# Optimization experiments

Measured on AMD Instinct MI355X. Metric: run time of the kernel, lower is better.

Reference implementation:

```python
import jax, jax.numpy as jnp
import numpy as np
import math

MODEL_DIM = 1024
B, S = 4, 2048


def setup_inputs() -> dict:
    key = jax.random.key(0)
    k_x, k_q, k_k, k_v = jax.random.split(key, 4)
    r5 = math.sqrt(5)
    x = jax.random.normal(k_x, (B, S, MODEL_DIM), dtype=jnp.float32)
    Q = jax.random.uniform(k_q, (MODEL_DIM, MODEL_DIM), minval=-r5, maxval=r5, dtype=jnp.float32)
    K = jax.random.uniform(k_k, (MODEL_DIM, MODEL_DIM), minval=-r5, maxval=r5, dtype=jnp.float32)
    V = jax.random.uniform(k_v, (MODEL_DIM, MODEL_DIM), minval=-r5, maxval=r5, dtype=jnp.float32)
    # attention_input == 'both' -> a == model_dim -> F is the full identity
    F = jnp.eye(MODEL_DIM, dtype=jnp.float32)
    return {"x": x, "Q": Q, "K": K, "V": V, "F": F}


def reference(x, Q, K, V, F):
    d = x.shape[-1]
    xf = jnp.matmul(x, F)
    Qx = jnp.matmul(xf, Q)          # [B,S,D]
    Kx = jnp.matmul(xf, K)          # [B,S,D]
    Vx = jnp.matmul(x, V)           # [B,S,D]
    scores = jnp.einsum('bqd,bkd->bqk', Qx, Kx) / math.sqrt(d)  # [B,S,S]
    seq = x.shape[1]
    mask = jnp.triu(jnp.ones((seq, seq), dtype=bool), k=1)
    scores = jnp.where(mask, -jnp.inf, scores)
    probs = jax.nn.softmax(scores, axis=-1)
    out = jnp.matmul(probs, Vx)     # [B,S,D]
    return (out, probs)
```

## Files before the change

### kernel.cpp

```cpp
#include <hip/hip_runtime.h>
#include <hip/hip_fp16.h>

typedef _Float16 f16;
typedef __attribute__((ext_vector_type(8))) _Float16 f16x8;
typedef __attribute__((ext_vector_type(4))) _Float16 f16x4;
typedef __attribute__((ext_vector_type(4))) float    f32x4;

#define D_MODEL 1024
#define SEQ     2048
#define BATCH   4
#define M_TOT   (BATCH * SEQ)
#define NE      ((long)M_TOT * D_MODEL)
#define WE      ((long)D_MODEL * D_MODEL)
#define OUT_ELEMS  ((long)M_TOT * D_MODEL)

static __device__ __forceinline__ f16x8 frag_read(const f16* lds, int row, int c)
{
    const f16x8* L = (const f16x8*)lds;
    return L[row * 4 + (c ^ ((row >> 1) & 3))];
}

static __device__ __forceinline__ void stage_tile(const f16* __restrict__ g, int row0,
                                                  int ld, int k0, f16* ldsbase,
                                                  int wave, int lane)
{
#pragma unroll
    for (int j = 0; j < 2; ++j) {
        const int chunk = wave * 2 + j;
        const int off16 = chunk * 64 + lane;
        const int row   = off16 >> 2;
        const int slot  = (off16 & 3) ^ ((row >> 1) & 3);
        const f16* src = g + (long)(row0 + row) * ld + (k0 + slot * 8);
        f16* dst = ldsbase + chunk * 512;
        __builtin_amdgcn_global_load_lds((const __attribute__((address_space(1))) void*)src,
                                         (__attribute__((address_space(3))) void*)dst,
                                         16, 0, 0);
    }
}

template<int ROWS>
static __device__ __forceinline__ void stage8(const f16* __restrict__ g, int row0,
                                              int ld, int k0, f16* dstbase,
                                              int wave, int lane)
{
#pragma unroll
    for (int j = 0; j < ROWS / 128; ++j) {
        const int off16 = j * 512 + wave * 64 + lane;
        const int row   = off16 >> 2;
        const int slot  = (off16 & 3) ^ ((row >> 1) & 3);
        const f16* src = g + (long)(row0 + row) * ld + (k0 + slot * 8);
        f16* dst = dstbase + (j * 512 + wave * 64) * 8;
        __builtin_amdgcn_global_load_lds((const __attribute__((address_space(1))) void*)src,
                                         (__attribute__((address_space(3))) void*)dst,
                                         16, 0, 0);
    }
}

#define BUFE 24576

template<int DUAL>
static __device__ __forceinline__ void g8_issueA(const f16* Ah, const f16* Al, int ld,
                                                 int m0, f16* lds, int t, int wave, int lane)
{
    f16* b = lds + (t & 1) * BUFE;
    stage8<256>(Ah, m0, ld, t * 32, b, wave, lane);
    if constexpr (DUAL) stage8<256>(Al, m0, ld, t * 32, b + 8192, wave, lane);
}
static __device__ __forceinline__ void g8_issueBh(const f16* BTh, int ld, int n0,
                                                  f16* lds, int t, int wave, int lane)
{
    stage8<128>(BTh, n0, ld, t * 32, lds + (t & 1) * BUFE + 16384, wave, lane);
}
static __device__ __forceinline__ void g8_issueBl(const f16* BTl, int ld, int n0,
                                                  f16* lds, int t, int wave, int lane)
{
    stage8<128>(BTl, n0, ld, t * 32, lds + (t & 1) * BUFE + 20480, wave, lane);
}

template<int DUAL>
static __device__ __forceinline__ void gemm8_pipe(
    const f16* __restrict__ Ah, const f16* __restrict__ Al,
    const f16* __restrict__ BTh, const f16* __restrict__ BTl,
    int ld, int m0, int n0, f16* lds, f32x4 acc[4][4], int wave, int lane)
{
    const int wr = wave >> 1, wc = wave & 1;
    const int cf = lane >> 4;

#pragma unroll
    for (int mi = 0; mi < 4; ++mi)
#pragma unroll
        for (int ni = 0; ni < 4; ++ni) acc[mi][ni] = (f32x4){0.f, 0.f, 0.f, 0.f};

    g8_issueA<DUAL>(Ah, Al, ld, m0, lds, 0, wave, lane);
    g8_issueBh(BTh, ld, n0, lds, 0, wave, lane);
    if constexpr (DUAL) g8_issueBl(BTl, ld, n0, lds, 0, wave, lane);
    g8_issueA<DUAL>(Ah, Al, ld, m0, lds, 1, wave, lane);
    g8_issueBh(BTh, ld, n0, lds, 1, wave, lane);

    for (int t = 0; t < 32; ++t) {
        if (t < 31) {
            if constexpr (DUAL) {
                g8_issueBl(BTl, ld, n0, lds, t + 1, wave, lane);
                asm volatile("s_waitcnt vmcnt(6)" ::: "memory");
            } else {
                asm volatile("s_waitcnt vmcnt(3)" ::: "memory");
            }
        } else {
            asm volatile("s_waitcnt vmcnt(0)" ::: "memory");
        }
        __builtin_amdgcn_sched_barrier(0);
        __builtin_amdgcn_s_barrier();
        __builtin_amdgcn_sched_barrier(0);

        f16* buf = lds + (t & 1) * BUFE;
        f16x8 fah[4], fal[4], fbh[4], fbl[4];
#pragma unroll
        for (int i = 0; i < 4; ++i) {
            const int ra = wr * 64 + i * 16 + (lane & 15);
            fah[i] = frag_read(buf, ra, cf);
            if constexpr (DUAL) fal[i] = frag_read(buf + 8192, ra, cf);
            const int rb = wc * 64 + i * 16 + (lane & 15);
            fbh[i] = frag_read(buf + 16384, rb, cf);
            if constexpr (DUAL) fbl[i] = frag_read(buf + 20480, rb, cf);
        }
        asm volatile("s_waitcnt lgkmcnt(0)" ::: "memory");
        __builtin_amdgcn_sched_barrier(0);
        __builtin_amdgcn_s_barrier();
        __builtin_amdgcn_sched_barrier(0);

        if (t < 30) {
            g8_issueA<DUAL>(Ah, Al, ld, m0, lds, t + 2, wave, lane);
            g8_issueBh(BTh, ld, n0, lds, t + 2, wave, lane);
        }
        __builtin_amdgcn_sched_barrier(0);

        __builtin_amdgcn_s_setprio(1);
#pragma unroll
        for (int mi = 0; mi < 4; ++mi)
#pragma unroll
            for (int ni = 0; ni < 4; ++ni)
                acc[mi][ni] = __builtin_amdgcn_mfma_f32_16x16x32_f16(fah[mi], fbh[ni], acc[mi][ni], 0, 0, 0);
        if constexpr (DUAL) {
#pragma unroll
            for (int mi = 0; mi < 4; ++mi)
#pragma unroll
                for (int ni = 0; ni < 4; ++ni)
                    acc[mi][ni] = __builtin_amdgcn_mfma_f32_16x16x32_f16(fah[mi], fbl[ni], acc[mi][ni], 0, 0, 0);
#pragma unroll
            for (int mi = 0; mi < 4; ++mi)
#pragma unroll
                for (int ni = 0; ni < 4; ++ni)
                    acc[mi][ni] = __builtin_amdgcn_mfma_f32_16x16x32_f16(fal[mi], fbh[ni], acc[mi][ni], 0, 0, 0);
        }
        __builtin_amdgcn_s_setprio(0);
    }
}

__global__ __launch_bounds__(512, 2) void k_gemm_T(
    const f16* __restrict__ xh, const f16* __restrict__ xl,
    const f16* __restrict__ WhT, const f16* __restrict__ WlT,
    f16* __restrict__ Th, f16* __restrict__ Tl)
{
    __shared__ __align__(16) f16 lds[49152];
    const int lane = threadIdx.x & 63, wave = threadIdx.x >> 6;
    const int L = blockIdx.x;
    const int swz = (L & 7) * 32 + (L >> 3);
    const int m0 = (swz >> 3) * 256;
    const int n0 = (swz & 7) * 128;
    f32x4 acc[4][4];
    gemm8_pipe<1>(xh, xl, WhT, WlT, D_MODEL, m0, n0, lds, acc, wave, lane);
    const int wr = wave >> 1, wc = wave & 1;
#pragma unroll
    for (int mi = 0; mi < 4; ++mi)
#pragma unroll
        for (int ni = 0; ni < 4; ++ni) {
            const int gn = n0 + wc * 64 + ni * 16 + (lane & 15);
#pragma unroll
            for (int r = 0; r < 4; ++r) {
                const int gm = m0 + wr * 64 + mi * 16 + (lane >> 4) * 4 + r;
                const float v = acc[mi][ni][r];
                const f16 h = (f16)v;
                Th[(long)gm * D_MODEL + gn] = h;
                Tl[(long)gm * D_MODEL + gn] = (f16)(v - (float)h);
            }
        }
}

__global__ __launch_bounds__(512, 2) void k_mega1(
    const f16* __restrict__ Th, const f16* __restrict__ Tl,
    const f16* __restrict__ xh, const f16* __restrict__ xl,
    const f16* __restrict__ VhT,
    float* __restrict__ scores, f16* __restrict__ VxT)
{
    __shared__ __align__(16) f16 lds[49152];
    const int lane = threadIdx.x & 63, wave = threadIdx.x >> 6;
    const int wr = wave >> 1, wc = wave & 1;
    f32x4 acc[4][4];

    if (blockIdx.x < 288) {
        const int L = blockIdx.x;
        const int swz = (L & 7) * 36 + (L >> 3);
        const int b = swz / 72;
        const int t = swz - b * 72;
        int qt = (int)((sqrtf(4.f * (float)t + 1.f) - 1.f) * 0.5f);
        while ((qt + 1) * (qt + 2) <= t) ++qt;
        while (qt * (qt + 1) > t) --qt;
        const int kt = t - qt * (qt + 1);

        const long ob = (long)b * SEQ * D_MODEL;
        gemm8_pipe<1>(Th + ob, Tl + ob, xh + ob, xl + ob, D_MODEL,
                      qt * 256, kt * 128, lds, acc, wave, lane);

        float* sb = scores + (long)b * SEQ * SEQ;
#pragma unroll
        for (int mi = 0; mi < 4; ++mi)
#pragma unroll
            for (int ni = 0; ni < 4; ++ni) {
                const int k = kt * 128 + wc * 64 + ni * 16 + (lane & 15);
#pragma unroll
                for (int r = 0; r < 4; ++r) {
                    const int q = qt * 256 + wr * 64 + mi * 16 + (lane >> 4) * 4 + r;
                    sb[(long)q * SEQ + k] = acc[mi][ni][r] * 0.03125f;
                }
            }
    } else {
        const int idx = blockIdx.x - 288;
        const int m0 = (idx >> 3) * 256;
        const int n0 = (idx & 7) * 128;
        gemm8_pipe<0>(xh, nullptr, VhT, nullptr, D_MODEL, m0, n0, lds, acc, wave, lane);
#pragma unroll
        for (int mi = 0; mi < 4; ++mi) {
            const int gm0 = m0 + wr * 64 + mi * 16 + (lane >> 4) * 4;
            const int b = gm0 >> 11, s = gm0 & 2047;
#pragma unroll
            for (int ni = 0; ni < 4; ++ni) {
                const int gn = n0 + wc * 64 + ni * 16 + (lane & 15);
                f16x4 p = {(f16)acc[mi][ni][0], (f16)acc[mi][ni][1],
                           (f16)acc[mi][ni][2], (f16)acc[mi][ni][3]};
                *(f16x4*)(VxT + ((long)b * D_MODEL + gn) * SEQ + s) = p;
            }
        }
    }
}

template<int DUAL>
static __device__ __forceinline__ void gemm_core(
    const f16* __restrict__ Ah, const f16* __restrict__ Al,
    const f16* __restrict__ BTh, const f16* __restrict__ BTl,
    int ld, int m0, int n0, int kEnd, f16* lds, f32x4 acc[4][4])
{
    const int t = threadIdx.x;
    const int lane = t & 63;
    const int wave = t >> 6;
    const int wr = wave >> 1, wc = wave & 1;
    const int cfrag = lane >> 4;

#pragma unroll
    for (int mi = 0; mi < 4; ++mi)
#pragma unroll
        for (int ni = 0; ni < 4; ++ni)
            acc[mi][ni] = (f32x4){0.f, 0.f, 0.f, 0.f};

    for (int k0 = 0; k0 < kEnd; k0 += 32) {
        stage_tile(Ah,  m0, ld, k0, lds,         wave, lane);
        stage_tile(BTh, n0, ld, k0, lds + 4096,  wave, lane);
        if (DUAL) {
            stage_tile(Al,  m0, ld, k0, lds + 8192,  wave, lane);
            stage_tile(BTl, n0, ld, k0, lds + 12288, wave, lane);
        }
        __syncthreads();

        f16x8 fah[4], fbh[4];
#pragma unroll
        for (int i = 0; i < 4; ++i) {
            fah[i] = frag_read(lds,        wr * 64 + i * 16 + (lane & 15), cfrag);
            fbh[i] = frag_read(lds + 4096, wc * 64 + i * 16 + (lane & 15), cfrag);
        }
        if (DUAL) {
            f16x8 fal[4], fbl[4];
#pragma unroll
            for (int i = 0; i < 4; ++i) {
                fal[i] = frag_read(lds + 8192,  wr * 64 + i * 16 + (lane & 15), cfrag);
                fbl[i] = frag_read(lds + 12288, wc * 64 + i * 16 + (lane & 15), cfrag);
            }
#pragma unroll
            for (int mi = 0; mi < 4; ++mi)
#pragma unroll
                for (int ni = 0; ni < 4; ++ni) {
                    acc[mi][ni] = __builtin_amdgcn_mfma_f32_16x16x32_f16(fah[mi], fbh[ni], acc[mi][ni], 0, 0, 0);
                    acc[mi][ni] = __builtin_amdgcn_mfma_f32_16x16x32_f16(fah[mi], fbl[ni], acc[mi][ni], 0, 0, 0);
                    acc[mi][ni] = __builtin_amdgcn_mfma_f32_16x16x32_f16(fal[mi], fbh[ni], acc[mi][ni], 0, 0, 0);
                }
        } else {
#pragma unroll
            for (int mi = 0; mi < 4; ++mi)
#pragma unroll
                for (int ni = 0; ni < 4; ++ni)
                    acc[mi][ni] = __builtin_amdgcn_mfma_f32_16x16x32_f16(fah[mi], fbh[ni], acc[mi][ni], 0, 0, 0);
        }
        __syncthreads();
    }
}

__global__ __launch_bounds__(256) void k_split_all(
    const float* __restrict__ x, const float* __restrict__ Q,
    const float* __restrict__ K, const float* __restrict__ V,
    f16* __restrict__ xh, f16* __restrict__ xl,
    f16* __restrict__ Qh, f16* __restrict__ Ql,
    f16* __restrict__ Kh, f16* __restrict__ Kl,
    f16* __restrict__ VhT)
{
    __shared__ float tile[32][33];
    const int bid = blockIdx.x;
    if (bid < 10240) {
        const float* src; f16 *dh, *dl; long off;
        if (bid < 8192)      { src = x; dh = xh; dl = xl; off = (long)bid * 1024; }
        else if (bid < 9216) { src = Q; dh = Qh; dl = Ql; off = (long)(bid - 8192) * 1024; }
        else                 { src = K; dh = Kh; dl = Kl; off = (long)(bid - 9216) * 1024; }
        const long i = off + threadIdx.x * 4;
        float4 v = *(const float4*)(src + i);
        f16 h0 = (f16)v.x, h1 = (f16)v.y, h2 = (f16)v.z, h3 = (f16)v.w;
        f16x4 hh = {h0, h1, h2, h3};
        f16x4 ll = {(f16)(v.x - (float)h0), (f16)(v.y - (float)h1),
                    (f16)(v.z - (float)h2), (f16)(v.w - (float)h3)};
        *(f16x4*)(dh + i) = hh;
        *(f16x4*)(dl + i) = ll;
    } else {
        const int idx = bid - 10240;
        const int n0 = (idx & 31) * 32, k0 = (idx >> 5) * 32;
        const int c = threadIdx.x & 31, r8 = threadIdx.x >> 5;
#pragma unroll
        for (int i = 0; i < 4; ++i) {
            const int r = r8 + i * 8;
            tile[r][c] = V[(long)(k0 + r) * D_MODEL + n0 + c];
        }
        __syncthreads();
#pragma unroll
        for (int i = 0; i < 4; ++i) {
            const int r = r8 + i * 8;
            VhT[(long)(n0 + r) * D_MODEL + k0 + c] = (f16)tile[c][r];
        }
    }
}

__global__ __launch_bounds__(256, 2) void k_gemm_w(
    const f16* __restrict__ Qh, const f16* __restrict__ Ql,
    const f16* __restrict__ Kh, const f16* __restrict__ Kl,
    f16* __restrict__ WhT, f16* __restrict__ WlT)
{
    __shared__ __align__(16) f16 lds[16384];
    f32x4 acc[4][4];
    const int m0 = blockIdx.y * 128, n0 = blockIdx.x * 128;
    gemm_core<1>(Qh, Ql, Kh, Kl, D_MODEL, m0, n0, D_MODEL, lds, acc);
    const int lane = threadIdx.x & 63, wave = threadIdx.x >> 6;
    const int wr = wave >> 1, wc = wave & 1;
#pragma unroll
    for (int mi = 0; mi < 4; ++mi)
#pragma unroll
        for (int ni = 0; ni < 4; ++ni) {
            const int gn = n0 + wc * 64 + ni * 16 + (lane & 15);
#pragma unroll
            for (int r = 0; r < 4; ++r) {
                const int gm = m0 + wr * 64 + mi * 16 + (lane >> 4) * 4 + r;
                const float v = acc[mi][ni][r];
                const f16 h = (f16)v;
                WhT[(long)gn * D_MODEL + gm] = h;
                WlT[(long)gn * D_MODEL + gm] = (f16)(v - (float)h);
            }
        }
}

__global__ __launch_bounds__(256) void k_softmax(float* __restrict__ probs,
                                                 f16* __restrict__ probs16)
{
    const long row = blockIdx.x;
    const int q = (int)(row & (SEQ - 1));
    float* s = probs + row * SEQ;
    const int t = threadIdx.x;
    const int kb = t * 8;
    float4 u0 = *(const float4*)(s + kb);
    float4 u1 = *(const float4*)(s + kb + 4);
    float v[8] = {u0.x, u0.y, u0.z, u0.w, u1.x, u1.y, u1.z, u1.w};
    float mx = -3.0e38f;
#pragma unroll
    for (int j = 0; j < 8; ++j) if (kb + j <= q) mx = fmaxf(mx, v[j]);
#pragma unroll
    for (int off = 32; off > 0; off >>= 1) mx = fmaxf(mx, __shfl_xor(mx, off, 64));
    __shared__ float redA[4], redB[4];
    const int lane = t & 63, wave = t >> 6;
    if (lane == 0) redA[wave] = mx;
    __syncthreads();
    mx = fmaxf(fmaxf(redA[0], redA[1]), fmaxf(redA[2], redA[3]));
    float e[8]; float sum = 0.f;
#pragma unroll
    for (int j = 0; j < 8; ++j) { e[j] = (kb + j <= q) ? __expf(v[j] - mx) : 0.f; sum += e[j]; }
#pragma unroll
    for (int off = 32; off > 0; off >>= 1) sum += __shfl_xor(sum, off, 64);
    if (lane == 0) redB[wave] = sum;
    __syncthreads();
    sum = (redB[0] + redB[1]) + (redB[2] + redB[3]);
    const float inv = 1.f / sum;
    float4 w0 = {e[0] * inv, e[1] * inv, e[2] * inv, e[3] * inv};
    float4 w1 = {e[4] * inv, e[5] * inv, e[6] * inv, e[7] * inv};
    *(float4*)(s + kb) = w0;
    *(float4*)(s + kb + 4) = w1;
    f16x8 p16 = {(f16)w0.x, (f16)w0.y, (f16)w0.z, (f16)w0.w,
                 (f16)w1.x, (f16)w1.y, (f16)w1.z, (f16)w1.w};
    *(f16x8*)(probs16 + row * SEQ + kb) = p16;
}

__global__ __launch_bounds__(256, 2) void k_gemm_pv(
    const f16* __restrict__ P, const f16* __restrict__ VT, float* __restrict__ out)
{
    const int dt = blockIdx.x, qt = 15 - blockIdx.y, b = blockIdx.z;
    __shared__ __align__(16) f16 lds[8192];
    f32x4 acc[4][4];
    const f16* Pb  = P  + (long)b * SEQ * SEQ;
    const f16* VTb = VT + (long)b * D_MODEL * SEQ;
    gemm_core<0>(Pb, nullptr, VTb, nullptr, SEQ, qt * 128, dt * 128, (qt + 1) * 128, lds, acc);
    float* ob = out + (long)b * SEQ * D_MODEL;
    const int lane = threadIdx.x & 63, wave = threadIdx.x >> 6;
    const int wr = wave >> 1, wc = wave & 1;
#pragma unroll
    for (int mi = 0; mi < 4; ++mi)
#pragma unroll
        for (int ni = 0; ni < 4; ++ni) {
            const int d = dt * 128 + wc * 64 + ni * 16 + (lane & 15);
#pragma unroll
            for (int r = 0; r < 4; ++r) {
                const int qq = qt * 128 + wr * 64 + mi * 16 + (lane >> 4) * 4 + r;
                ob[(long)qq * D_MODEL + d] = acc[mi][ni][r];
            }
        }
}

extern "C" void kernel_launch(void* const* d_in, const int* in_sizes, int n_in,
                              void* d_out, int out_size, void* d_ws, size_t ws_size,
                              hipStream_t stream)
{
    const float* x = (const float*)d_in[0];
    const float* Q = (const float*)d_in[1];
    const float* K = (const float*)d_in[2];
    const float* V = (const float*)d_in[3];

    float* out   = (float*)d_out;
    float* probs = out + OUT_ELEMS;

    f16* base = (f16*)d_ws;
    f16* xh   = base;
    f16* xl   = base + NE;
    f16* Th   = base + 2 * NE;
    f16* Tl   = base + 3 * NE;
    f16* VxT  = base + 4 * NE;
    f16* Qh   = base + 5 * NE;
    f16* Ql   = Qh + WE;
    f16* Kh   = Qh + 2 * WE;
    f16* Kl   = Qh + 3 * WE;
    f16* WhT  = Qh + 4 * WE;
    f16* WlT  = Qh + 5 * WE;
    f16* VhT  = Qh + 6 * WE;
    f16* probs16 = base + 2 * NE;

    k_split_all<<<11264, 256, 0, stream>>>(x, Q, K, V, xh, xl, Qh, Ql, Kh, Kl, VhT);
    k_gemm_w<<<dim3(8, 8), 256, 0, stream>>>(Qh, Ql, Kh, Kl, WhT, WlT);
    k_gemm_T<<<256, 512, 0, stream>>>(xh, xl, WhT, WlT, Th, Tl);
    k_mega1<<<544, 512, 0, stream>>>(Th, Tl, xh, xl, VhT, probs, VxT);
    k_softmax<<<8192, 256, 0, stream>>>(probs, probs16);
    k_gemm_pv<<<dim3(8, 16, 4), 256, 0, stream>>>(probs16, VxT, out);
}
```

Measured before the change: 274.3 us.

## Use 256x256 score tiles and pipelined 256x128 PV GEMM

The dual-precision scores GEMM in the mega kernel now uses 256x256 tiles, giving 144 causal blocks instead of 288 with 128-wide tiles. Each block reuses its staged fragments across more MFMAs, at the cost of 128 KB of LDS and more accumulator registers. The P·V GEMM moves from the simple 128x128 single-buffer core to the double-buffered 8-wave gemm8_pipe, which now takes a variable causal K-tile count. Larger tiles may lower occupancy and worsen load balance across the causal triangle.

After: 259.0 us. 5.6% less time.

```diff
diff --git a/kernel.cpp b/kernel.cpp
--- a/kernel.cpp
+++ b/kernel.cpp
@@ -81,7 +81,7 @@
 static __device__ __forceinline__ void gemm8_pipe(
     const f16* __restrict__ Ah, const f16* __restrict__ Al,
     const f16* __restrict__ BTh, const f16* __restrict__ BTl,
-    int ld, int m0, int n0, f16* lds, f32x4 acc[4][4], int wave, int lane)
+    int ld, int m0, int n0, int nT, f16* lds, f32x4 acc[4][4], int wave, int lane)
 {
     const int wr = wave >> 1, wc = wave & 1;
     const int cf = lane >> 4;
@@ -97,8 +97,8 @@
     g8_issueA<DUAL>(Ah, Al, ld, m0, lds, 1, wave, lane);
     g8_issueBh(BTh, ld, n0, lds, 1, wave, lane);
 
-    for (int t = 0; t < 32; ++t) {
-        if (t < 31) {
+    for (int t = 0; t < nT; ++t) {
+        if (t < nT - 1) {
             if constexpr (DUAL) {
                 g8_issueBl(BTl, ld, n0, lds, t + 1, wave, lane);
                 asm volatile("s_waitcnt vmcnt(6)" ::: "memory");
@@ -128,7 +128,7 @@
         __builtin_amdgcn_s_barrier();
         __builtin_amdgcn_sched_barrier(0);
 
-        if (t < 30) {
+        if (t < nT - 2) {
             g8_issueA<DUAL>(Ah, Al, ld, m0, lds, t + 2, wave, lane);
             g8_issueBh(BTh, ld, n0, lds, t + 2, wave, lane);
         }
@@ -152,6 +152,94 @@
                 for (int ni = 0; ni < 4; ++ni)
                     acc[mi][ni] = __builtin_amdgcn_mfma_f32_16x16x32_f16(fal[mi], fbh[ni], acc[mi][ni], 0, 0, 0);
         }
+        __builtin_amdgcn_s_setprio(0);
+    }
+}
+
+#define BUFE2 32768
+
+static __device__ __forceinline__ void g256_main(const f16* Ah, const f16* Al,
+                                                 const f16* BTh, int ld, int m0, int n0,
+                                                 f16* lds, int t, int wave, int lane)
+{
+    f16* b = lds + (t & 1) * BUFE2;
+    stage8<256>(Ah,  m0, ld, t * 32, b,         wave, lane);
+    stage8<256>(Al,  m0, ld, t * 32, b + 8192,  wave, lane);
+    stage8<256>(BTh, n0, ld, t * 32, b + 16384, wave, lane);
+}
+static __device__ __forceinline__ void g256_bl(const f16* BTl, int ld, int n0,
+                                               f16* lds, int t, int wave, int lane)
+{
+    stage8<256>(BTl, n0, ld, t * 32, lds + (t & 1) * BUFE2 + 24576, wave, lane);
+}
+
+static __device__ __forceinline__ void gemm256d(
+    const f16* __restrict__ Ah, const f16* __restrict__ Al,
+    const f16* __restrict__ BTh, const f16* __restrict__ BTl,
+    int ld, int m0, int n0, f16* lds, f32x4 acc[8][4], int wave, int lane)
+{
+    const int wr = wave >> 2, wc = wave & 3;
+    const int cf = lane >> 4;
+
+#pragma unroll
+    for (int mi = 0; mi < 8; ++mi)
+#pragma unroll
+        for (int ni = 0; ni < 4; ++ni) acc[mi][ni] = (f32x4){0.f, 0.f, 0.f, 0.f};
+
+    g256_main(Ah, Al, BTh, ld, m0, n0, lds, 0, wave, lane);
+    g256_bl(BTl, ld, n0, lds, 0, wave, lane);
+    g256_main(Ah, Al, BTh, ld, m0, n0, lds, 1, wave, lane);
+
+    for (int t = 0; t < 32; ++t) {
+        if (t < 31) {
+            g256_bl(BTl, ld, n0, lds, t + 1, wave, lane);
+            asm volatile("s_waitcnt vmcnt(8)" ::: "memory");
+        } else {
+            asm volatile("s_waitcnt vmcnt(0)" ::: "memory");
+        }
+        __builtin_amdgcn_sched_barrier(0);
+        __builtin_amdgcn_s_barrier();
+        __builtin_amdgcn_sched_barrier(0);
+
+        f16* buf = lds + (t & 1) * BUFE2;
+        f16x8 fah[8], fal[8], fbh[4], fbl[4];
+#pragma unroll
+        for (int mi = 0; mi < 8; ++mi) {
+            const int ra = wr * 128 + mi * 16 + (lane & 15);
+            fah[mi] = frag_read(buf,        ra, cf);
+            fal[mi] = frag_read(buf + 8192, ra, cf);
+        }
+#pragma unroll
+        for (int ni = 0; ni < 4; ++ni) {
+            const int rb = wc * 64 + ni * 16 + (lane & 15);
+            fbh[ni] = frag_read(buf + 16384, rb, cf);
+            fbl[ni] = frag_read(buf + 24576, rb, cf);
+        }
+        asm volatile("s_waitcnt lgkmcnt(0)" ::: "memory");
+        __builtin_amdgcn_sched_barrier(0);
+        __builtin_amdgcn_s_barrier();
+        __builtin_amdgcn_sched_barrier(0);
+
+        if (t < 30)
+            g256_main(Ah, Al, BTh, ld, m0, n0, lds, t + 2, wave, lane);
+        __builtin_amdgcn_sched_barrier(0);
+
+        __builtin_amdgcn_s_setprio(1);
+#pragma unroll
+        for (int mi = 0; mi < 8; ++mi)
+#pragma unroll
+            for (int ni = 0; ni < 4; ++ni)
+                acc[mi][ni] = __builtin_amdgcn_mfma_f32_16x16x32_f16(fah[mi], fbh[ni], acc[mi][ni], 0, 0, 0);
+#pragma unroll
+        for (int mi = 0; mi < 8; ++mi)
+#pragma unroll
+            for (int ni = 0; ni < 4; ++ni)
+                acc[mi][ni] = __builtin_amdgcn_mfma_f32_16x16x32_f16(fah[mi], fbl[ni], acc[mi][ni], 0, 0, 0);
+#pragma unroll
+        for (int mi = 0; mi < 8; ++mi)
+#pragma unroll
+            for (int ni = 0; ni < 4; ++ni)
+                acc[mi][ni] = __builtin_amdgcn_mfma_f32_16x16x32_f16(fal[mi], fbh[ni], acc[mi][ni], 0, 0, 0);
         __builtin_amdgcn_s_setprio(0);
     }
 }
@@ -168,7 +256,7 @@
     const int m0 = (swz >> 3) * 256;
     const int n0 = (swz & 7) * 128;
     f32x4 acc[4][4];
-    gemm8_pipe<1>(xh, xl, WhT, WlT, D_MODEL, m0, n0, lds, acc, wave, lane);
+    gemm8_pipe<1>(xh, xl, WhT, WlT, D_MODEL, m0, n0, 32, lds, acc, wave, lane);
     const int wr = wave >> 1, wc = wave & 1;
 #pragma unroll
     for (int mi = 0; mi < 4; ++mi)
@@ -192,42 +280,43 @@
     const f16* __restrict__ VhT,
     float* __restrict__ scores, f16* __restrict__ VxT)
 {
-    __shared__ __align__(16) f16 lds[49152];
+    __shared__ __align__(16) f16 lds[65536];
     const int lane = threadIdx.x & 63, wave = threadIdx.x >> 6;
-    const int wr = wave >> 1, wc = wave & 1;
-    f32x4 acc[4][4];
-
-    if (blockIdx.x < 288) {
+
+    if (blockIdx.x < 144) {
         const int L = blockIdx.x;
-        const int swz = (L & 7) * 36 + (L >> 3);
-        const int b = swz / 72;
-        const int t = swz - b * 72;
-        int qt = (int)((sqrtf(4.f * (float)t + 1.f) - 1.f) * 0.5f);
-        while ((qt + 1) * (qt + 2) <= t) ++qt;
-        while (qt * (qt + 1) > t) --qt;
-        const int kt = t - qt * (qt + 1);
+        const int b = L / 36;
+        const int t = L - b * 36;
+        int qt = (int)((sqrtf(8.f * (float)t + 1.f) - 1.f) * 0.5f);
+        while ((qt + 1) * (qt + 2) / 2 <= t) ++qt;
+        while (qt * (qt + 1) / 2 > t) --qt;
+        const int kt = t - qt * (qt + 1) / 2;
 
         const long ob = (long)b * SEQ * D_MODEL;
-        gemm8_pipe<1>(Th + ob, Tl + ob, xh + ob, xl + ob, D_MODEL,
-                      qt * 256, kt * 128, lds, acc, wave, lane);
+        f32x4 acc[8][4];
+        gemm256d(Th + ob, Tl + ob, xh + ob, xl + ob, D_MODEL,
+                 qt * 256, kt * 256, lds, acc, wave, lane);
 
         float* sb = scores + (long)b * SEQ * SEQ;
-#pragma unroll
-        for (int mi = 0; mi < 4; ++mi)
+        const int wr = wave >> 2, wc = wave & 3;
+#pragma unroll
+        for (int mi = 0; mi < 8; ++mi)
 #pragma unroll
             for (int ni = 0; ni < 4; ++ni) {
-                const int k = kt * 128 + wc * 64 + ni * 16 + (lane & 15);
+                const int k = kt * 256 + wc * 64 + ni * 16 + (lane & 15);
 #pragma unroll
                 for (int r = 0; r < 4; ++r) {
-                    const int q = qt * 256 + wr * 64 + mi * 16 + (lane >> 4) * 4 + r;
+                    const int q = qt * 256 + wr * 128 + mi * 16 + (lane >> 4) * 4 + r;
                     sb[(long)q * SEQ + k] = acc[mi][ni][r] * 0.03125f;
                 }
             }
     } else {
-        const int idx = blockIdx.x - 288;
+        const int idx = blockIdx.x - 144;
         const int m0 = (idx >> 3) * 256;
         const int n0 = (idx & 7) * 128;
-        gemm8_pipe<0>(xh, nullptr, VhT, nullptr, D_MODEL, m0, n0, lds, acc, wave, lane);
+        f32x4 acc[4][4];
+        gemm8_pipe<0>(xh, nullptr, VhT, nullptr, D_MODEL, m0, n0, 32, lds, acc, wave, lane);
+        const int wr = wave >> 1, wc = wave & 1;
 #pragma unroll
         for (int mi = 0; mi < 4; ++mi) {
             const int gm0 = m0 + wr * 64 + mi * 16 + (lane >> 4) * 4;
@@ -243,8 +332,36 @@
     }
 }
 
-template<int DUAL>
-static __device__ __forceinline__ void gemm_core(
+__global__ __launch_bounds__(512, 2) void k_gemm_pv8(
+    const f16* __restrict__ P, const f16* __restrict__ VT, float* __restrict__ out)
+{
+    __shared__ __align__(16) f16 lds[49152];
+    const int lane = threadIdx.x & 63, wave = threadIdx.x >> 6;
+    const int i = blockIdx.x;
+    const int qt = 7 - (i >> 5);
+    const int dt = (i >> 2) & 7;
+    const int b  = i & 3;
+    const int nT = 8 * (qt + 1);
+    f32x4 acc[4][4];
+    const f16* Pb  = P  + (long)b * SEQ * SEQ;
+    const f16* VTb = VT + (long)b * D_MODEL * SEQ;
+    gemm8_pipe<0>(Pb, nullptr, VTb, nullptr, SEQ, qt * 256, dt * 128, nT, lds, acc, wave, lane);
+    float* ob = out + (long)b * SEQ * D_MODEL;
+    const int wr = wave >> 1, wc = wave & 1;
+#pragma unroll
+    for (int mi = 0; mi < 4; ++mi)
+#pragma unroll
+        for (int ni = 0; ni < 4; ++ni) {
+            const int d = dt * 128 + wc * 64 + ni * 16 + (lane & 15);
+#pragma unroll
+            for (int r = 0; r < 4; ++r) {
+                const int qq = qt * 256 + wr * 64 + mi * 16 + (lane >> 4) * 4 + r;
+                ob[(long)qq * D_MODEL + d] = acc[mi][ni][r];
+            }
+        }
+}
+
+static __device__ __forceinline__ void gemm_core_dual(
     const f16* __restrict__ Ah, const f16* __restrict__ Al,
     const f16* __restrict__ BTh, const f16* __restrict__ BTl,
     int ld, int m0, int n0, int kEnd, f16* lds, f32x4 acc[4][4])
@@ -264,40 +381,26 @@
     for (int k0 = 0; k0 < kEnd; k0 += 32) {
         stage_tile(Ah,  m0, ld, k0, lds,         wave, lane);
         stage_tile(BTh, n0, ld, k0, lds + 4096,  wave, lane);
-        if (DUAL) {
-            stage_tile(Al,  m0, ld, k0, lds + 8192,  wave, lane);
-            stage_tile(BTl, n0, ld, k0, lds + 12288, wave, lane);
-        }
+        stage_tile(Al,  m0, ld, k0, lds + 8192,  wave, lane);
+        stage_tile(BTl, n0, ld, k0, lds + 12288, wave, lane);
         __syncthreads();
 
-        f16x8 fah[4], fbh[4];
+        f16x8 fah[4], fbh[4], fal[4], fbl[4];
 #pragma unroll
         for (int i = 0; i < 4; ++i) {
-            fah[i] = frag_read(lds,        wr * 64 + i * 16 + (lane & 15), cfrag);
-            fbh[i] = frag_read(lds + 4096, wc * 64 + i * 16 + (lane & 15), cfrag);
-        }
-        if (DUAL) {
-            f16x8 fal[4], fbl[4];
-#pragma unroll
-            for (int i = 0; i < 4; ++i) {
-                fal[i] = frag_read(lds + 8192,  wr * 64 + i * 16 + (lane & 15), cfrag);
-                fbl[i] = frag_read(lds + 12288, wc * 64 + i * 16 + (lane & 15), cfrag);
-            }
-#pragma unroll
-            for (int mi = 0; mi < 4; ++mi)
-#pragma unroll
-                for (int ni = 0; ni < 4; ++ni) {
-                    acc[mi][ni] = __builtin_amdgcn_mfma_f32_16x16x32_f16(fah[mi], fbh[ni], acc[mi][ni], 0, 0, 0);
-                    acc[mi][ni] = __builtin_amdgcn_mfma_f32_16x16x32_f16(fah[mi], fbl[ni], acc[mi][ni], 0, 0, 0);
-                    acc[mi][ni] = __builtin_amdgcn_mfma_f32_16x16x32_f16(fal[mi], fbh[ni], acc[mi][ni], 0, 0, 0);
-                }
-        } else {
-#pragma unroll
-            for (int mi = 0; mi < 4; ++mi)
-#pragma unroll
-                for (int ni = 0; ni < 4; ++ni)
-                    acc[mi][ni] = __builtin_amdgcn_mfma_f32_16x16x32_f16(fah[mi], fbh[ni], acc[mi][ni], 0, 0, 0);
-        }
+            fah[i] = frag_read(lds,         wr * 64 + i * 16 + (lane & 15), cfrag);
+            fbh[i] = frag_read(lds + 4096,  wc * 64 + i * 16 + (lane & 15), cfrag);
+            fal[i] = frag_read(lds + 8192,  wr * 64 + i * 16 + (lane & 15), cfrag);
+            fbl[i] = frag_read(lds + 12288, wc * 64 + i * 16 + (lane & 15), cfrag);
+        }
+#pragma unroll
+        for (int mi = 0; mi < 4; ++mi)
+#pragma unroll
+            for (int ni = 0; ni < 4; ++ni) {
+                acc[mi][ni] = __builtin_amdgcn_mfma_f32_16x16x32_f16(fah[mi], fbh[ni], acc[mi][ni], 0, 0, 0);
+                acc[mi][ni] = __builtin_amdgcn_mfma_f32_16x16x32_f16(fah[mi], fbl[ni], acc[mi][ni], 0, 0, 0);
+                acc[mi][ni] = __builtin_amdgcn_mfma_f32_16x16x32_f16(fal[mi], fbh[ni], acc[mi][ni], 0, 0, 0);
+            }
         __syncthreads();
     }
 }
@@ -351,7 +454,7 @@
     __shared__ __align__(16) f16 lds[16384];
     f32x4 acc[4][4];
     const int m0 = blockIdx.y * 128, n0 = blockIdx.x * 128;
-    gemm_core<1>(Qh, Ql, Kh, Kl, D_MODEL, m0, n0, D_MODEL, lds, acc);
+    gemm_core_dual(Qh, Ql, Kh, Kl, D_MODEL, m0, n0, D_MODEL, lds, acc);
     const int lane = threadIdx.x & 63, wave = threadIdx.x >> 6;
     const int wr = wave >> 1, wc = wave & 1;
 #pragma unroll
@@ -407,31 +510,6 @@
     f16x8 p16 = {(f16)w0.x, (f16)w0.y, (f16)w0.z, (f16)w0.w,
                  (f16)w1.x, (f16)w1.y, (f16)w1.z, (f16)w1.w};
     *(f16x8*)(probs16 + row * SEQ + kb) = p16;
-}
-
-__global__ __launch_bounds__(256, 2) void k_gemm_pv(
-    const f16* __restrict__ P, const f16* __restrict__ VT, float* __restrict__ out)
-{
-    const int dt = blockIdx.x, qt = 15 - blockIdx.y, b = blockIdx.z;
-    __shared__ __align__(16) f16 lds[8192];
-    f32x4 acc[4][4];
-    const f16* Pb  = P  + (long)b * SEQ * SEQ;
-    const f16* VTb = VT + (long)b * D_MODEL * SEQ;
-    gemm_core<0>(Pb, nullptr, VTb, nullptr, SEQ, qt * 128, dt * 128, (qt + 1) * 128, lds, acc);
-    float* ob = out + (long)b * SEQ * D_MODEL;
-    const int lane = threadIdx.x & 63, wave = threadIdx.x >> 6;
-    const int wr = wave >> 1, wc = wave & 1;
-#pragma unroll
-    for (int mi = 0; mi < 4; ++mi)
-#pragma unroll
-        for (int ni = 0; ni < 4; ++ni) {
-            const int d = dt * 128 + wc * 64 + ni * 16 + (lane & 15);
-#pragma unroll
-            for (int r = 0; r < 4; ++r) {
-                const int qq = qt * 128 + wr * 64 + mi * 16 + (lane >> 4) * 4 + r;
-                ob[(long)qq * D_MODEL + d] = acc[mi][ni][r];
-            }
-        }
 }
 
 extern "C" void kernel_launch(void* const* d_in, const int* in_sizes, int n_in,
@@ -464,7 +542,7 @@
     k_split_all<<<11264, 256, 0, stream>>>(x, Q, K, V, xh, xl, Qh, Ql, Kh, Kl, VhT);
     k_gemm_w<<<dim3(8, 8), 256, 0, stream>>>(Qh, Ql, Kh, Kl, WhT, WlT);
     k_gemm_T<<<256, 512, 0, stream>>>(xh, xl, WhT, WlT, Th, Tl);
-    k_mega1<<<544, 512, 0, stream>>>(Th, Tl, xh, xl, VhT, probs, VxT);
+    k_mega1<<<400, 512, 0, stream>>>(Th, Tl, xh, xl, VhT, probs, VxT);
     k_softmax<<<8192, 256, 0, stream>>>(probs, probs16);
-    k_gemm_pv<<<dim3(8, 16, 4), 256, 0, stream>>>(probs16, VxT, out);
-}
+    k_gemm_pv8<<<256, 512, 0, stream>>>(probs16, VxT, out);
+}
```
